# Kernel optimization log

Hardware: AMD Instinct MI355X
Metric: run time of the kernel (lower is better)

## Reference

```python
import jax, jax.numpy as jnp
import numpy as np

V, SMAX, D, L, H, F = 50257, 1024, 768, 12, 12, 3072
DH = D // H
SCALE = float(np.sqrt(DH))


def setup_inputs() -> dict:
    key = jax.random.key(0)
    ks = jax.random.split(key, 24)
    B, S = 2, 1024
    std = 0.02
    inp = {
        'input_ids': jax.random.randint(ks[0], (B, S), 0, V),
        'tok_emb': jax.random.normal(ks[1], (V, D), jnp.float32) * std,
        'pos_emb': jax.random.normal(ks[2], (SMAX, D), jnp.float32) * std,
        # stacked per-layer params (leading dim L)
        'Wq': jax.random.normal(ks[3], (L, D, D), jnp.float32) * std,
        'bq': jnp.zeros((L, D), jnp.float32),
        'Wk': jax.random.normal(ks[4], (L, D, D), jnp.float32) * std,
        'bk': jnp.zeros((L, D), jnp.float32),
        'Wv': jax.random.normal(ks[5], (L, D, D), jnp.float32) * std,
        'bv': jnp.zeros((L, D), jnp.float32),
        'Wo': jax.random.normal(ks[6], (L, D, D), jnp.float32) * std,
        'bo': jnp.zeros((L, D), jnp.float32),
        'ln1_g': jnp.ones((L, D), jnp.float32),
        'ln1_b': jnp.zeros((L, D), jnp.float32),
        'ln2_g': jnp.ones((L, D), jnp.float32),
        'ln2_b': jnp.zeros((L, D), jnp.float32),
        'W1': jax.random.normal(ks[7], (L, D, F), jnp.float32) * std,
        'b1': jnp.zeros((L, F), jnp.float32),
        'W2': jax.random.normal(ks[8], (L, F, D), jnp.float32) * std,
        'b2': jnp.zeros((L, D), jnp.float32),
        'lnf_g': jnp.ones((D,), jnp.float32),
        'lnf_b': jnp.zeros((D,), jnp.float32),
        'Whead': jax.random.normal(ks[9], (D, V), jnp.float32) * std,
    }
    return inp


def _layernorm(x, g, b, eps=1e-5):
    mu = jnp.mean(x, axis=-1, keepdims=True)
    var = jnp.var(x, axis=-1, keepdims=True)
    return (x - mu) * jax.lax.rsqrt(var + eps) * g + b


def _gpt_forward(input_ids, tok_emb, pos_emb, Wq, bq, Wk, bk, Wv, bv, Wo, bo,
                 ln1_g, ln1_b, ln2_g, ln2_b, W1, b1, W2, b2, lnf_g, lnf_b, Whead):
    B, S = input_ids.shape
    x = tok_emb[input_ids] + pos_emb[:S][None, :, :]  # (B,S,D)
    # additive causal mask: -inf above the diagonal
    idx = jnp.arange(S)
    neg_inf = jnp.finfo(x.dtype).min
    mask = jnp.where(idx[None, :] > idx[:, None], neg_inf, 0.0).astype(x.dtype)  # (S,S)

    def block(x, p):
        (wq, bq_, wk, bk_, wv, bv_, wo, bo_, g1, b1_, g2, b2_, w1, bb1, w2, bb2) = p
        h = _layernorm(x, g1, b1_)
        q = (h @ wq + bq_).reshape(B, S, H, DH)
        k = (h @ wk + bk_).reshape(B, S, H, DH)
        v = (h @ wv + bv_).reshape(B, S, H, DH)
        scores = jnp.einsum('bqhd,bkhd->bhqk', q, k) / SCALE + mask
        attn = jax.nn.softmax(scores, axis=-1)
        o = jnp.einsum('bhqk,bkhd->bqhd', attn, v).reshape(B, S, D)
        x = x + (o @ wo + bo_)
        h2 = _layernorm(x, g2, b2_)
        ffn = jax.nn.gelu(h2 @ w1 + bb1, approximate=False) @ w2 + bb2
        return x + ffn, None

    params = (Wq, bq, Wk, bk, Wv, bv, Wo, bo, ln1_g, ln1_b, ln2_g, ln2_b, W1, b1, W2, b2)
    x, _ = jax.lax.scan(block, x, params)
    x = _layernorm(x, lnf_g, lnf_b)
    return x @ Whead  # (B,S,V) logits


def reference(input_ids, tok_emb, pos_emb, Wq, bq, Wk, bk, Wv, bv, Wo, bo,
              ln1_g, ln1_b, ln2_g, ln2_b, W1, b1, W2, b2, lnf_g, lnf_b, Whead):
    return _gpt_forward(input_ids, tok_emb, pos_emb, Wq, bq, Wk, bk, Wv, bv, Wo, bo,
                        ln1_g, ln1_b, ln2_g, ln2_b, W1, b1, W2, b2, lnf_g, lnf_b, Whead)
```

## Files before the change

kernel.cpp:

```cpp
#include <hip/hip_runtime.h>
#include <hip/hip_bf16.h>
#include <cstdint>
#include <cstddef>

#define DEV __device__ __forceinline__

typedef __attribute__((ext_vector_type(8))) short short8;
typedef __attribute__((ext_vector_type(4))) float f32x4;
typedef unsigned short u16;
typedef unsigned int u32;

static constexpr int Vv = 50257;
static constexpr int Dd = 768;
static constexpr int Ll = 12;
static constexpr int Hh = 12;
static constexpr int Ff = 3072;
static constexpr int Ss = 1024;
static constexpr int Bbatch = 2;
static constexpr int DHh = 64;
static constexpr int Mtok = Bbatch * Ss;
static constexpr int NQKV = 3 * Dd;
static constexpr int VPAD = 50304;

DEV float bf2f(u16 u){ u32 x = ((u32)u) << 16; float f; __builtin_memcpy(&f, &x, 4); return f; }
DEV u16 f2bf(float f){ u32 x; __builtin_memcpy(&x, &f, 4); x += 0x7fffu + ((x >> 16) & 1u); return (u16)(x >> 16); }

DEV void gld_lds16(const void* g, void* l){
  __builtin_amdgcn_global_load_lds((const __attribute__((address_space(1))) void*)g,
                                   (__attribute__((address_space(3))) void*)l, 16, 0, 0);
}

__global__ void k_embed(const int* __restrict__ ids, const float* __restrict__ tok,
                        const float* __restrict__ pos, float* __restrict__ x){
  int t = blockIdx.x;
  int id = ids[t];
  int s = t & (Ss - 1);
  const float* tr = tok + (size_t)id * Dd;
  const float* pr = pos + (size_t)s * Dd;
  float* xr = x + (size_t)t * Dd;
  for (int c = threadIdx.x; c < Dd; c += blockDim.x) xr[c] = tr[c] + pr[c];
}

__global__ __launch_bounds__(256) void k_ln(const float* __restrict__ x, const float* __restrict__ g,
                                            const float* __restrict__ b, u16* __restrict__ y){
  int row = blockIdx.x, tid = threadIdx.x;
  const float* xr = x + (size_t)row * Dd;
  float v0 = xr[tid], v1 = xr[tid + 256], v2 = xr[tid + 512];
  float s = v0 + v1 + v2, ss = v0 * v0 + v1 * v1 + v2 * v2;
  for (int o = 1; o < 64; o <<= 1){ s += __shfl_xor(s, o, 64); ss += __shfl_xor(ss, o, 64); }
  __shared__ float red[8];
  int w = tid >> 6, l = tid & 63;
  if (l == 0){ red[w] = s; red[w + 4] = ss; }
  __syncthreads();
  s = red[0] + red[1] + red[2] + red[3];
  ss = red[4] + red[5] + red[6] + red[7];
  float mu = s * (1.0f / Dd);
  float var = ss * (1.0f / Dd) - mu * mu;
  float rs = rsqrtf(var + 1e-5f);
  u16* yr = y + (size_t)row * Dd;
  yr[tid]       = f2bf((v0 - mu) * rs * g[tid]       + b[tid]);
  yr[tid + 256] = f2bf((v1 - mu) * rs * g[tid + 256] + b[tid + 256]);
  yr[tid + 512] = f2bf((v2 - mu) * rs * g[tid + 512] + b[tid + 512]);
}

__global__ void k_transpose(const float* __restrict__ src, u16* __restrict__ dst,
                            int R, int C, long smat, long dmat){
  __shared__ float tile[32][33];
  src += (size_t)blockIdx.z * smat;
  dst += (size_t)blockIdx.z * dmat;
  int c0 = blockIdx.x * 32, r0 = blockIdx.y * 32;
  int tx = threadIdx.x, ty = threadIdx.y;
  #pragma unroll
  for (int i = 0; i < 4; i++){
    int r = r0 + ty + i * 8, c = c0 + tx;
    if (c < C) tile[ty + i * 8][tx] = src[(size_t)r * C + c];
  }
  __syncthreads();
  #pragma unroll
  for (int i = 0; i < 4; i++){
    int c = c0 + ty + i * 8, r = r0 + tx;
    if (c < C) dst[(size_t)c * R + r] = f2bf(tile[tx][ty + i * 8]);
  }
}

__global__ void k_vt(const u16* __restrict__ qkv, u16* __restrict__ vt){
  __shared__ u16 tile[32][33];
  int z = blockIdx.z, b = z / Hh, h = z % Hh;
  int d0 = blockIdx.x * 32, s0 = blockIdx.y * 32;
  int tx = threadIdx.x, ty = threadIdx.y;
  #pragma unroll
  for (int i = 0; i < 4; i++){
    int sP = s0 + ty + i * 8;
    tile[ty + i * 8][tx] = qkv[(size_t)(b * Ss + sP) * NQKV + 2 * Dd + h * DHh + d0 + tx];
  }
  __syncthreads();
  #pragma unroll
  for (int i = 0; i < 4; i++){
    int d = d0 + ty + i * 8;
    vt[((size_t)(z * DHh + d)) * Ss + s0 + tx] = tile[tx][ty + i * 8];
  }
}

__global__ void k_biaspack(const float* __restrict__ bq, const float* __restrict__ bk,
                           const float* __restrict__ bv, float* __restrict__ o){
  int i = blockIdx.x * 256 + threadIdx.x;
  int col = i % NQKV, lay = i / NQKV;
  float v = (col < Dd) ? bq[lay * Dd + col]
          : (col < 2 * Dd) ? bk[lay * Dd + col - Dd]
          : bv[lay * Dd + col - 2 * Dd];
  o[i] = v;
}

__global__ __launch_bounds__(256) void k_combine(const float* __restrict__ p,
                                                 const float* __restrict__ bias,
                                                 float* __restrict__ x){
  int i = blockIdx.x * 256 + threadIdx.x;
  f32x4 a  = ((const f32x4*)x)[i];
  f32x4 q0 = ((const f32x4*)p)[i];
  f32x4 q1 = ((const f32x4*)(p + (size_t)Mtok * Dd))[i];
  int col0 = (i * 4) % Dd;
  f32x4 bv = *(const f32x4*)(bias + col0);
  ((f32x4*)x)[i] = a + q0 + q1 + bv;
}

template<int BM, int BN, int ACT, bool RES, bool OUTBF, bool SCALEQ, bool NB, bool HASBIAS, bool SPLIT>
__global__ __launch_bounds__(256) void k_gemm(const u16* __restrict__ A, const u16* __restrict__ Bt,
                                              const float* __restrict__ bias, const float* __restrict__ res,
                                              float* __restrict__ Cf, u16* __restrict__ Cb,
                                              int Mm, int Nn, int Kk, int MT, int NT, int KS){
  constexpr int HM = BM / 2, HN = BN / 2;
  constexpr int FM = HM / 16, FN = HN / 16;
  __shared__ __align__(16) u16 ldsA[2][BM * 32];
  __shared__ __align__(16) u16 ldsB[2][BN * 32];
  int tid = threadIdx.x, wid = tid >> 6, l = tid & 63;
  int wm = wid >> 1, wn = wid & 1;
  int lr = l & 15, lc = l >> 4;
  int nwg = gridDim.x, dIdx = blockIdx.x;
  int L = ((nwg & 7) == 0) ? ((dIdx & 7) * (nwg >> 3) + (dIdx >> 3)) : dIdx;
  int kidx = 0;
  if (SPLIT){ int per = MT * NT; kidx = L / per; L -= kidx * per; }
  int mtile = L % MT, ntile = L / MT;
  int m0 = mtile * BM, n0 = ntile * BN;
  int klen = Kk / KS, kbase = kidx * klen, nk = klen >> 5;

  f32x4 acc[FM][FN];
  #pragma unroll
  for (int i = 0; i < FM; i++)
    #pragma unroll
    for (int j = 0; j < FN; j++) acc[i][j] = (f32x4)0.0f;

  constexpr int nA = (BM * 4) / 256, nB = (BN * 4) / 256;
  auto stage = [&](int buf, int kk){
    #pragma unroll
    for (int i = 0; i < nA; i++){
      int id = i * 256 + tid, row = id >> 2, c = id & 3;
      int cs = c ^ ((row >> 1) & 3);
      gld_lds16(A + (size_t)(m0 + row) * Kk + kk + cs * 8,
                (char*)ldsA[buf] + (size_t)(i * 256 + (wid << 6)) * 16);
    }
    #pragma unroll
    for (int i = 0; i < nB; i++){
      int id = i * 256 + tid, row = id >> 2, c = id & 3;
      int cs = c ^ ((row >> 1) & 3);
      gld_lds16(Bt + (size_t)(n0 + row) * Kk + kk + cs * 8,
                (char*)ldsB[buf] + (size_t)(i * 256 + (wid << 6)) * 16);
    }
  };
  auto compute = [&](int buf){
    short8 af[FM], bfr[FN];
    #pragma unroll
    for (int i = 0; i < FM; i++){
      int row = wm * HM + i * 16 + lr;
      af[i] = *(const short8*)((const char*)ldsA[buf] + row * 64 + ((lc ^ ((row >> 1) & 3)) << 4));
    }
    #pragma unroll
    for (int j = 0; j < FN; j++){
      int row = wn * HN + j * 16 + lr;
      bfr[j] = *(const short8*)((const char*)ldsB[buf] + row * 64 + ((lc ^ ((row >> 1) & 3)) << 4));
    }
    #pragma unroll
    for (int i = 0; i < FM; i++)
      #pragma unroll
      for (int j = 0; j < FN; j++)
        acc[i][j] = __builtin_amdgcn_mfma_f32_16x16x32_bf16(af[i], bfr[j], acc[i][j], 0, 0, 0);
  };

  stage(0, kbase);
  __syncthreads();
  for (int t = 0; t < nk - 1; ++t){
    stage((t + 1) & 1, kbase + (t + 1) * 32);
    compute(t & 1);
    __syncthreads();
  }
  compute((nk - 1) & 1);

  if (SPLIT){
    float* P = Cf + (size_t)kidx * Mm * Nn;
    #pragma unroll
    for (int i = 0; i < FM; i++)
      #pragma unroll
      for (int j = 0; j < FN; j++){
        int col = n0 + wn * HN + j * 16 + lr;
        #pragma unroll
        for (int r = 0; r < 4; r++){
          int row = m0 + wm * HM + i * 16 + lc * 4 + r;
          P[(size_t)row * Nn + col] = acc[i][j][r];
        }
      }
    return;
  }
  #pragma unroll
  for (int i = 0; i < FM; i++){
    #pragma unroll
    for (int j = 0; j < FN; j++){
      int col = n0 + wn * HN + j * 16 + lr;
      if (NB && col >= Nn) continue;
      float bv = HASBIAS ? bias[col] : 0.0f;
      #pragma unroll
      for (int r = 0; r < 4; r++){
        int row = m0 + wm * HM + i * 16 + lc * 4 + r;
        float v = acc[i][j][r] + bv;
        if (SCALEQ){ if (col < Dd) v *= 0.125f; }
        if (ACT == 1) v = 0.5f * v * (1.0f + erff(v * 0.70710678118f));
        if (RES) v += res[(size_t)row * Nn + col];
        if (OUTBF) Cb[(size_t)row * Nn + col] = f2bf(v);
        else       Cf[(size_t)row * Nn + col] = v;
      }
    }
  }
}

__global__ __launch_bounds__(256) void k_attn(const u16* __restrict__ qkv, const u16* __restrict__ vt,
                                              u16* __restrict__ o){
  __shared__ __align__(16) u16 ldsK[64 * 64];
  __shared__ __align__(16) u16 ldsV[64 * 64];
  __shared__ __align__(16) u16 ldsP[4 * 16 * 72];
  int iq = blockIdx.x, bh = blockIdx.y, b = bh / Hh, h = bh % Hh;
  int tid = threadIdx.x, wid = tid >> 6, l = tid & 63, lr = l & 15, lc = l >> 4;
  int qrow = b * Ss + iq * 64 + wid * 16 + lr;
  const u16* qp = qkv + (size_t)qrow * NQKV + h * DHh;
  short8 qf[2];
  qf[0] = *(const short8*)(qp + lc * 8);
  qf[1] = *(const short8*)(qp + 32 + lc * 8);
  float mreg[4], lsum[4];
  f32x4 oacc[4];
  #pragma unroll
  for (int r = 0; r < 4; r++){ mreg[r] = -1e30f; lsum[r] = 0.0f; }
  #pragma unroll
  for (int i = 0; i < 4; i++) oacc[i] = (f32x4)0.0f;
  u16* pbase = ldsP + wid * 16 * 72;
  for (int j = 0; j <= iq; j++){
    #pragma unroll
    for (int c = 0; c < 2; c++){
      int id = c * 256 + tid, row = id >> 3, ch = id & 7;
      int cs = ch ^ (row & 7);
      gld_lds16(qkv + (size_t)(b * Ss + j * 64 + row) * NQKV + Dd + h * DHh + cs * 8,
                (char*)ldsK + (size_t)(c * 256 + (wid << 6)) * 16);
      gld_lds16(vt + ((size_t)(bh * DHh + row)) * Ss + j * 64 + cs * 8,
                (char*)ldsV + (size_t)(c * 256 + (wid << 6)) * 16);
    }
    __syncthreads();
    f32x4 sc[4];
    #pragma unroll
    for (int fn = 0; fn < 4; fn++) sc[fn] = (f32x4)0.0f;
    #pragma unroll
    for (int fn = 0; fn < 4; fn++){
      int kv = fn * 16 + lr;
      #pragma unroll
      for (int ks = 0; ks < 2; ks++){
        int ch = ks * 4 + lc;
        short8 kf = *(const short8*)((const char*)ldsK + kv * 128 + ((ch ^ (kv & 7)) << 4));
        sc[fn] = __builtin_amdgcn_mfma_f32_16x16x32_bf16(qf[ks], kf, sc[fn], 0, 0, 0);
      }
    }
    if (j == iq){
      #pragma unroll
      for (int fn = 0; fn < 4; fn++){
        int kv = fn * 16 + lr;
        #pragma unroll
        for (int r = 0; r < 4; r++){
          int qr = wid * 16 + lc * 4 + r;
          if (kv > qr) sc[fn][r] = -1e30f;
        }
      }
    }
    float alpha[4];
    #pragma unroll
    for (int r = 0; r < 4; r++){
      float mx = fmaxf(fmaxf(sc[0][r], sc[1][r]), fmaxf(sc[2][r], sc[3][r]));
      mx = fmaxf(mx, __shfl_xor(mx, 1, 64));
      mx = fmaxf(mx, __shfl_xor(mx, 2, 64));
      mx = fmaxf(mx, __shfl_xor(mx, 4, 64));
      mx = fmaxf(mx, __shfl_xor(mx, 8, 64));
      float mnew = fmaxf(mreg[r], mx);
      alpha[r] = __expf(mreg[r] - mnew);
      mreg[r] = mnew;
      float rsum = 0.0f;
      #pragma unroll
      for (int fn = 0; fn < 4; fn++){
        float p = __expf(sc[fn][r] - mnew);
        sc[fn][r] = p;
        rsum += p;
      }
      rsum += __shfl_xor(rsum, 1, 64);
      rsum += __shfl_xor(rsum, 2, 64);
      rsum += __shfl_xor(rsum, 4, 64);
      rsum += __shfl_xor(rsum, 8, 64);
      lsum[r] = lsum[r] * alpha[r] + rsum;
    }
    #pragma unroll
    for (int fn = 0; fn < 4; fn++)
      #pragma unroll
      for (int r = 0; r < 4; r++)
        pbase[(lc * 4 + r) * 72 + fn * 16 + lr] = f2bf(sc[fn][r]);
    #pragma unroll
    for (int fd = 0; fd < 4; fd++)
      #pragma unroll
      for (int r = 0; r < 4; r++) oacc[fd][r] *= alpha[r];
    short8 pa[2];
    #pragma unroll
    for (int ks = 0; ks < 2; ks++)
      pa[ks] = *(const short8*)((const char*)pbase + lr * 144 + (ks * 4 + lc) * 16);
    #pragma unroll
    for (int fd = 0; fd < 4; fd++){
      int dd = fd * 16 + lr;
      #pragma unroll
      for (int ks = 0; ks < 2; ks++){
        int ch = ks * 4 + lc;
        short8 vf = *(const short8*)((const char*)ldsV + dd * 128 + ((ch ^ (dd & 7)) << 4));
        oacc[fd] = __builtin_amdgcn_mfma_f32_16x16x32_bf16(pa[ks], vf, oacc[fd], 0, 0, 0);
      }
    }
    __syncthreads();
  }
  #pragma unroll
  for (int fd = 0; fd < 4; fd++)
    #pragma unroll
    for (int r = 0; r < 4; r++){
      int row = b * Ss + iq * 64 + wid * 16 + lc * 4 + r;
      o[(size_t)row * Dd + h * DHh + fd * 16 + lr] = f2bf(oacc[fd][r] / lsum[r]);
    }
}

extern "C" void kernel_launch(void* const* d_in, const int* in_sizes, int n_in,
                              void* d_out, int out_size, void* d_ws, size_t ws_size,
                              hipStream_t stream){
  const int*   ids  = (const int*)d_in[0];
  const float* tok  = (const float*)d_in[1];
  const float* pos  = (const float*)d_in[2];
  const float* Wq   = (const float*)d_in[3];
  const float* bq   = (const float*)d_in[4];
  const float* Wk   = (const float*)d_in[5];
  const float* bk   = (const float*)d_in[6];
  const float* Wv   = (const float*)d_in[7];
  const float* bv   = (const float*)d_in[8];
  const float* Wo   = (const float*)d_in[9];
  const float* bo   = (const float*)d_in[10];
  const float* ln1g = (const float*)d_in[11];
  const float* ln1b = (const float*)d_in[12];
  const float* ln2g = (const float*)d_in[13];
  const float* ln2b = (const float*)d_in[14];
  const float* W1   = (const float*)d_in[15];
  const float* b1   = (const float*)d_in[16];
  const float* W2   = (const float*)d_in[17];
  const float* b2   = (const float*)d_in[18];
  const float* lnfg = (const float*)d_in[19];
  const float* lnfb = (const float*)d_in[20];
  const float* Wh   = (const float*)d_in[21];
  float* out = (float*)d_out;

  auto al = [](size_t x){ return (x + 255) & ~(size_t)255; };
  size_t off = 0;
  auto take = [&](size_t bytes){ size_t r = off; off = al(off + bytes); return r; };
  size_t o_x    = take((size_t)Mtok * Dd * 4);
  size_t o_h    = take((size_t)Mtok * Dd * 2);
  size_t o_qkv  = take((size_t)Mtok * NQKV * 2);
  size_t o_vt   = take((size_t)Bbatch * Hh * DHh * Ss * 2);
  size_t o_o    = take((size_t)Mtok * Dd * 2);
  size_t o_mid  = take((size_t)Mtok * Ff * 2);
  size_t o_bq   = take((size_t)Ll * NQKV * 4);
  size_t o_part = take((size_t)2 * Mtok * Dd * 4);
  size_t o_rot = off;
  size_t o_wqkv, o_wo, o_w1, o_w2, o_wh;
  bool full;
  {
    size_t t = off;
    o_wqkv = t; t = al(t + (size_t)Ll * NQKV * Dd * 2);
    o_wo   = t; t = al(t + (size_t)Ll * Dd * Dd * 2);
    o_w1   = t; t = al(t + (size_t)Ll * Ff * Dd * 2);
    o_w2   = t; t = al(t + (size_t)Ll * Dd * Ff * 2);
    o_wh   = t; t = al(t + (size_t)VPAD * Dd * 2);
    full = (t <= ws_size);
  }
  char* ws = (char*)d_ws;
  float* x    = (float*)(ws + o_x);
  u16*   h    = (u16*)(ws + o_h);
  u16*   qkvb = (u16*)(ws + o_qkv);
  u16*   vtb  = (u16*)(ws + o_vt);
  u16*   ob   = (u16*)(ws + o_o);
  u16*   midb = (u16*)(ws + o_mid);
  float* bqkvp= (float*)(ws + o_bq);
  float* part = (float*)(ws + o_part);
  u16* wqkvT = full ? (u16*)(ws + o_wqkv) : (u16*)(ws + o_rot);
  u16* woT   = full ? (u16*)(ws + o_wo)   : (u16*)(ws + o_rot);
  u16* w1T   = full ? (u16*)(ws + o_w1)   : (u16*)(ws + o_rot);
  u16* w2T   = full ? (u16*)(ws + o_w2)   : (u16*)(ws + o_rot);
  u16* whT   = full ? (u16*)(ws + o_wh)   : (u16*)(ws + o_rot);

  dim3 tb(32, 8);
  auto tpose = [&](const float* src, u16* dst, int R, int C, int nmat, long smat, long dmat){
    k_transpose<<<dim3((C + 31) / 32, R / 32, nmat), tb, 0, stream>>>(src, dst, R, C, smat, dmat);
  };

  k_biaspack<<<(Ll * NQKV) / 256, 256, 0, stream>>>(bq, bk, bv, bqkvp);
  k_embed<<<Mtok, 256, 0, stream>>>(ids, tok, pos, x);

  if (full){
    tpose(Wq, wqkvT,              Dd, Dd, Ll, (long)Dd * Dd, (long)NQKV * Dd);
    tpose(Wk, wqkvT + Dd * Dd,    Dd, Dd, Ll, (long)Dd * Dd, (long)NQKV * Dd);
    tpose(Wv, wqkvT + 2 * Dd * Dd,Dd, Dd, Ll, (long)Dd * Dd, (long)NQKV * Dd);
    tpose(Wo, woT, Dd, Dd, Ll, (long)Dd * Dd, (long)Dd * Dd);
    tpose(W1, w1T, Dd, Ff, Ll, (long)Dd * Ff, (long)Ff * Dd);
    tpose(W2, w2T, Ff, Dd, Ll, (long)Ff * Dd, (long)Dd * Ff);
    tpose(Wh, whT, Dd, Vv, 1, 0, 0);
  }

  auto gemm_qkv = [&](const u16* A, const u16* Bt, const float* bias, u16* Cb){
    constexpr int MT = Mtok / 64, NT = NQKV / 128;
    k_gemm<64, 128, 0, false, true, true, false, true, false>
      <<<MT * NT, 256, 0, stream>>>(A, Bt, bias, nullptr, nullptr, Cb, Mtok, NQKV, Dd, MT, NT, 1);
  };
  auto gemm_wo = [&](const u16* A, const u16* Bt, const float* bias, float* C){
    constexpr int MT = Mtok / 64, NT = Dd / 64;
    k_gemm<64, 64, 0, true, false, false, false, true, false>
      <<<MT * NT, 256, 0, stream>>>(A, Bt, bias, C, C, nullptr, Mtok, Dd, Dd, MT, NT, 1);
  };
  auto gemm_ffn1 = [&](const u16* A, const u16* Bt, const float* bias, u16* Cb){
    constexpr int MT = Mtok / 64, NT = Ff / 128;
    k_gemm<64, 128, 1, false, true, false, false, true, false>
      <<<MT * NT, 256, 0, stream>>>(A, Bt, bias, nullptr, nullptr, Cb, Mtok, Ff, Dd, MT, NT, 1);
  };
  auto gemm_ffn2 = [&](const u16* A, const u16* Bt){
    constexpr int MT = Mtok / 64, NT = Dd / 64;
    k_gemm<64, 64, 0, false, false, false, false, false, true>
      <<<MT * NT * 2, 256, 0, stream>>>(A, Bt, nullptr, nullptr, part, nullptr, Mtok, Dd, Ff, MT, NT, 2);
  };
  auto gemm_head = [&](const u16* A, const u16* Bt, float* C){
    constexpr int MT = Mtok / 128, NT = VPAD / 128;
    k_gemm<128, 128, 0, false, false, false, true, false, false>
      <<<MT * NT, 256, 0, stream>>>(A, Bt, nullptr, nullptr, C, nullptr, Mtok, Vv, Dd, MT, NT, 1);
  };

  for (int l = 0; l < Ll; ++l){
    const u16* wqkvL = full ? wqkvT + (size_t)l * NQKV * Dd : wqkvT;
    const u16* woL   = full ? woT   + (size_t)l * Dd * Dd   : woT;
    const u16* w1L   = full ? w1T   + (size_t)l * Ff * Dd   : w1T;
    const u16* w2L   = full ? w2T   + (size_t)l * Dd * Ff   : w2T;
    if (!full){
      tpose(Wq + (size_t)l * Dd * Dd, wqkvT,              Dd, Dd, 1, 0, 0);
      tpose(Wk + (size_t)l * Dd * Dd, wqkvT + Dd * Dd,    Dd, Dd, 1, 0, 0);
      tpose(Wv + (size_t)l * Dd * Dd, wqkvT + 2 * Dd * Dd,Dd, Dd, 1, 0, 0);
    }
    k_ln<<<Mtok, 256, 0, stream>>>(x, ln1g + l * Dd, ln1b + l * Dd, h);
    gemm_qkv(h, wqkvL, bqkvp + l * NQKV, qkvb);
    k_vt<<<dim3(2, 32, Bbatch * Hh), tb, 0, stream>>>(qkvb, vtb);
    k_attn<<<dim3(Ss / 64, Bbatch * Hh), 256, 0, stream>>>(qkvb, vtb, ob);
    if (!full) tpose(Wo + (size_t)l * Dd * Dd, woT, Dd, Dd, 1, 0, 0);
    gemm_wo(ob, woL, bo + l * Dd, x);
    k_ln<<<Mtok, 256, 0, stream>>>(x, ln2g + l * Dd, ln2b + l * Dd, h);
    if (!full) tpose(W1 + (size_t)l * Dd * Ff, w1T, Dd, Ff, 1, 0, 0);
    gemm_ffn1(h, w1L, b1 + l * Ff, midb);
    if (!full) tpose(W2 + (size_t)l * Ff * Dd, w2T, Ff, Dd, 1, 0, 0);
    gemm_ffn2(midb, w2L);
    k_combine<<<(Mtok * Dd / 4) / 256, 256, 0, stream>>>(part, b2 + l * Dd, x);
  }
  k_ln<<<Mtok, 256, 0, stream>>>(x, lnfg, lnfb, h);
  if (!full) tpose(Wh, whT, Dd, Vv, 1, 0, 0);
  gemm_head(h, whT, out);
}
```

Measured before the change: 2.235 ms.

## Add 4-stage pipelined GEMM kernel and fuse V transpose into QKV epilogue

Introduces a new GEMM kernel with a 4-deep LDS buffer ring, explicit vmcnt waits, one barrier per k-step, and split MFMA issue with priority hints. It is used for the QKV, FFN1 and LM-head GEMMs, with larger tiles (128x128, and 256x256 with 8 waves for the head). The V transpose kernel is removed: the QKV epilogue now also writes V in transposed layout, saving a launch and a read pass. The risks are more LDS per block, which can lower occupancy, and scattered transposed stores in the epilogue. The vocab padding is enlarged to fit the 256 tile, which assumes the head weight buffer is allocated for the larger padding.

```diff
diff --git a/kernel.cpp b/kernel.cpp
--- a/kernel.cpp
+++ b/kernel.cpp
@@ -4,6 +4,7 @@
 #include <cstddef>
 
 #define DEV __device__ __forceinline__
+#define WAITV(N) asm volatile("s_waitcnt vmcnt(" #N ")" ::: "memory")
 
 typedef __attribute__((ext_vector_type(8))) short short8;
 typedef __attribute__((ext_vector_type(4))) float f32x4;
@@ -20,7 +21,7 @@
 static constexpr int DHh = 64;
 static constexpr int Mtok = Bbatch * Ss;
 static constexpr int NQKV = 3 * Dd;
-static constexpr int VPAD = 50304;
+static constexpr int VPAD = 50432;
 
 DEV float bf2f(u16 u){ u32 x = ((u32)u) << 16; float f; __builtin_memcpy(&f, &x, 4); return f; }
 DEV u16 f2bf(float f){ u32 x; __builtin_memcpy(&x, &f, 4); x += 0x7fffu + ((x >> 16) & 1u); return (u16)(x >> 16); }
@@ -83,24 +84,6 @@
   }
 }
 
-__global__ void k_vt(const u16* __restrict__ qkv, u16* __restrict__ vt){
-  __shared__ u16 tile[32][33];
-  int z = blockIdx.z, b = z / Hh, h = z % Hh;
-  int d0 = blockIdx.x * 32, s0 = blockIdx.y * 32;
-  int tx = threadIdx.x, ty = threadIdx.y;
-  #pragma unroll
-  for (int i = 0; i < 4; i++){
-    int sP = s0 + ty + i * 8;
-    tile[ty + i * 8][tx] = qkv[(size_t)(b * Ss + sP) * NQKV + 2 * Dd + h * DHh + d0 + tx];
-  }
-  __syncthreads();
-  #pragma unroll
-  for (int i = 0; i < 4; i++){
-    int d = d0 + ty + i * 8;
-    vt[((size_t)(z * DHh + d)) * Ss + s0 + tx] = tile[tx][ty + i * 8];
-  }
-}
-
 __global__ void k_biaspack(const float* __restrict__ bq, const float* __restrict__ bk,
                            const float* __restrict__ bv, float* __restrict__ o){
   int i = blockIdx.x * 256 + threadIdx.x;
@@ -123,10 +106,134 @@
   ((f32x4*)x)[i] = a + q0 + q1 + bv;
 }
 
-template<int BM, int BN, int ACT, bool RES, bool OUTBF, bool SCALEQ, bool NB, bool HASBIAS, bool SPLIT>
+template<int BM, int BN, int NW, int EPI>
+__global__ __launch_bounds__(NW * 64, 2) void k_gemm8(
+    const u16* __restrict__ A, const u16* __restrict__ Bt,
+    const float* __restrict__ bias, float* __restrict__ Cf, u16* __restrict__ Cb,
+    u16* __restrict__ vt, int Nn, int Kk, int MT, int NT){
+  constexpr int NTHR = NW * 64;
+  constexpr int WM = 2, WN = NW / 2;
+  constexpr int WMS = BM / WM, WNS = BN / WN;
+  constexpr int FM = WMS / 16, FN = WNS / 16, FMH = FM / 2;
+  __shared__ __align__(16) u16 ldsA[4 * BM * 32];
+  __shared__ __align__(16) u16 ldsB[4 * BN * 32];
+  int tid = threadIdx.x, wid = tid >> 6, l = tid & 63;
+  int wm = wid / WN, wn = wid % WN;
+  int lr = l & 15, lc = l >> 4;
+  int nwg = gridDim.x, dIdx = blockIdx.x;
+  int L = (dIdx & 7) * (nwg >> 3) + (dIdx >> 3);
+  int mtile = L % MT, ntile = L / MT;
+  int m0 = mtile * BM, n0 = ntile * BN;
+
+  f32x4 acc[FM][FN];
+  #pragma unroll
+  for (int i = 0; i < FM; i++)
+    #pragma unroll
+    for (int j = 0; j < FN; j++) acc[i][j] = (f32x4)0.0f;
+
+  constexpr int nA = (BM * 4) / NTHR, nB = (BN * 4) / NTHR;
+  auto stage = [&](int buf, int kk){
+    char* dA = (char*)ldsA + buf * (BM * 64);
+    #pragma unroll
+    for (int i = 0; i < nA; i++){
+      int id = i * NTHR + tid, row = id >> 2, c = id & 3;
+      int cs = c ^ ((row >> 1) & 3);
+      gld_lds16(A + (size_t)(m0 + row) * Kk + kk + cs * 8, dA + (size_t)id * 16);
+    }
+    char* dB = (char*)ldsB + buf * (BN * 64);
+    #pragma unroll
+    for (int i = 0; i < nB; i++){
+      int id = i * NTHR + tid, row = id >> 2, c = id & 3;
+      int cs = c ^ ((row >> 1) & 3);
+      gld_lds16(Bt + (size_t)(n0 + row) * Kk + kk + cs * 8, dB + (size_t)id * 16);
+    }
+  };
+  auto compute = [&](int t){
+    const char* bA = (const char*)ldsA + (t & 3) * (BM * 64);
+    const char* bB = (const char*)ldsB + (t & 3) * (BN * 64);
+    short8 bfr[FN], af[FMH];
+    #pragma unroll
+    for (int j = 0; j < FN; j++){
+      int row = wn * WNS + j * 16 + lr;
+      bfr[j] = *(const short8*)(bB + row * 64 + ((lc ^ ((row >> 1) & 3)) << 4));
+    }
+    #pragma unroll
+    for (int i = 0; i < FMH; i++){
+      int row = wm * WMS + i * 16 + lr;
+      af[i] = *(const short8*)(bA + row * 64 + ((lc ^ ((row >> 1) & 3)) << 4));
+    }
+    asm volatile("s_waitcnt lgkmcnt(0)" ::: "memory");
+    __builtin_amdgcn_sched_barrier(0);
+    __builtin_amdgcn_s_setprio(1);
+    #pragma unroll
+    for (int i = 0; i < FMH; i++)
+      #pragma unroll
+      for (int j = 0; j < FN; j++)
+        acc[i][j] = __builtin_amdgcn_mfma_f32_16x16x32_bf16(af[i], bfr[j], acc[i][j], 0, 0, 0);
+    __builtin_amdgcn_s_setprio(0);
+    #pragma unroll
+    for (int i = 0; i < FMH; i++){
+      int row = wm * WMS + (FMH + i) * 16 + lr;
+      af[i] = *(const short8*)(bA + row * 64 + ((lc ^ ((row >> 1) & 3)) << 4));
+    }
+    asm volatile("s_waitcnt lgkmcnt(0)" ::: "memory");
+    __builtin_amdgcn_sched_barrier(0);
+    __builtin_amdgcn_s_setprio(1);
+    #pragma unroll
+    for (int i = 0; i < FMH; i++)
+      #pragma unroll
+      for (int j = 0; j < FN; j++)
+        acc[FMH + i][j] = __builtin_amdgcn_mfma_f32_16x16x32_bf16(af[i], bfr[j], acc[FMH + i][j], 0, 0, 0);
+    __builtin_amdgcn_s_setprio(0);
+  };
+
+  int nk = Kk >> 5;
+  stage(0, 0); stage(1, 32); stage(2, 64);
+  #pragma unroll 1
+  for (int t = 0; t < nk - 3; ++t){
+    WAITV(8);
+    __builtin_amdgcn_s_barrier();
+    __builtin_amdgcn_sched_barrier(0);
+    stage((t + 3) & 3, (t + 3) << 5);
+    compute(t);
+  }
+  WAITV(8); __builtin_amdgcn_s_barrier(); __builtin_amdgcn_sched_barrier(0); compute(nk - 3);
+  WAITV(4); __builtin_amdgcn_s_barrier(); __builtin_amdgcn_sched_barrier(0); compute(nk - 2);
+  WAITV(0); __builtin_amdgcn_s_barrier(); __builtin_amdgcn_sched_barrier(0); compute(nk - 1);
+
+  #pragma unroll
+  for (int i = 0; i < FM; i++){
+    #pragma unroll
+    for (int j = 0; j < FN; j++){
+      int col = n0 + wn * WNS + j * 16 + lr;
+      if (EPI == 0 && col >= Nn) continue;
+      float bv = (EPI != 0) ? bias[col] : 0.0f;
+      #pragma unroll
+      for (int r = 0; r < 4; r++){
+        int row = m0 + wm * WMS + i * 16 + lc * 4 + r;
+        float v = acc[i][j][r] + bv;
+        if (EPI == 1){ if (col < Dd) v *= 0.125f; }
+        if (EPI == 2) v = 0.5f * v * (1.0f + erff(v * 0.70710678118f));
+        if (EPI == 0){
+          Cf[(size_t)row * Nn + col] = v;
+        } else {
+          u16 bvv = f2bf(v);
+          Cb[(size_t)row * Nn + col] = bvv;
+          if (EPI == 1 && col >= 2 * Dd){
+            int c2 = col - 2 * Dd, hh = c2 >> 6, dd2 = c2 & 63;
+            int bb = row >> 10, ss2 = row & 1023;
+            vt[((size_t)((bb * Hh + hh) * DHh + dd2) << 10) + ss2] = bvv;
+          }
+        }
+      }
+    }
+  }
+}
+
+template<int BM, int BN, bool RES, bool SPLIT>
 __global__ __launch_bounds__(256) void k_gemm(const u16* __restrict__ A, const u16* __restrict__ Bt,
                                               const float* __restrict__ bias, const float* __restrict__ res,
-                                              float* __restrict__ Cf, u16* __restrict__ Cb,
+                                              float* __restrict__ Cf,
                                               int Mm, int Nn, int Kk, int MT, int NT, int KS){
   constexpr int HM = BM / 2, HN = BN / 2;
   constexpr int FM = HM / 16, FN = HN / 16;
@@ -156,14 +263,14 @@
       int id = i * 256 + tid, row = id >> 2, c = id & 3;
       int cs = c ^ ((row >> 1) & 3);
       gld_lds16(A + (size_t)(m0 + row) * Kk + kk + cs * 8,
-                (char*)ldsA[buf] + (size_t)(i * 256 + (wid << 6)) * 16);
+                (char*)ldsA[buf] + (size_t)id * 16);
     }
     #pragma unroll
     for (int i = 0; i < nB; i++){
       int id = i * 256 + tid, row = id >> 2, c = id & 3;
       int cs = c ^ ((row >> 1) & 3);
       gld_lds16(Bt + (size_t)(n0 + row) * Kk + kk + cs * 8,
-                (char*)ldsB[buf] + (size_t)(i * 256 + (wid << 6)) * 16);
+                (char*)ldsB[buf] + (size_t)id * 16);
     }
   };
   auto compute = [&](int buf){
@@ -214,17 +321,13 @@
     #pragma unroll
     for (int j = 0; j < FN; j++){
       int col = n0 + wn * HN + j * 16 + lr;
-      if (NB && col >= Nn) continue;
-      float bv = HASBIAS ? bias[col] : 0.0f;
+      float bv = bias[col];
       #pragma unroll
       for (int r = 0; r < 4; r++){
         int row = m0 + wm * HM + i * 16 + lc * 4 + r;
         float v = acc[i][j][r] + bv;
-        if (SCALEQ){ if (col < Dd) v *= 0.125f; }
-        if (ACT == 1) v = 0.5f * v * (1.0f + erff(v * 0.70710678118f));
         if (RES) v += res[(size_t)row * Nn + col];
-        if (OUTBF) Cb[(size_t)row * Nn + col] = f2bf(v);
-        else       Cf[(size_t)row * Nn + col] = v;
+        Cf[(size_t)row * Nn + col] = v;
       }
     }
   }
@@ -425,30 +528,25 @@
     tpose(Wh, whT, Dd, Vv, 1, 0, 0);
   }
 
-  auto gemm_qkv = [&](const u16* A, const u16* Bt, const float* bias, u16* Cb){
-    constexpr int MT = Mtok / 64, NT = NQKV / 128;
-    k_gemm<64, 128, 0, false, true, true, false, true, false>
-      <<<MT * NT, 256, 0, stream>>>(A, Bt, bias, nullptr, nullptr, Cb, Mtok, NQKV, Dd, MT, NT, 1);
-  };
-  auto gemm_wo = [&](const u16* A, const u16* Bt, const float* bias, float* C){
+  auto gemm_qkv = [&](const u16* Aop, const u16* Bop, const float* bias, u16* Cb){
+    constexpr int MT = Mtok / 128, NT = NQKV / 128;
+    k_gemm8<128, 128, 4, 1><<<MT * NT, 256, 0, stream>>>(Aop, Bop, bias, nullptr, Cb, vtb, NQKV, Dd, MT, NT);
+  };
+  auto gemm_wo = [&](const u16* Aop, const u16* Bop, const float* bias, float* C){
     constexpr int MT = Mtok / 64, NT = Dd / 64;
-    k_gemm<64, 64, 0, true, false, false, false, true, false>
-      <<<MT * NT, 256, 0, stream>>>(A, Bt, bias, C, C, nullptr, Mtok, Dd, Dd, MT, NT, 1);
-  };
-  auto gemm_ffn1 = [&](const u16* A, const u16* Bt, const float* bias, u16* Cb){
-    constexpr int MT = Mtok / 64, NT = Ff / 128;
-    k_gemm<64, 128, 1, false, true, false, false, true, false>
-      <<<MT * NT, 256, 0, stream>>>(A, Bt, bias, nullptr, nullptr, Cb, Mtok, Ff, Dd, MT, NT, 1);
-  };
-  auto gemm_ffn2 = [&](const u16* A, const u16* Bt){
+    k_gemm<64, 64, true, false><<<MT * NT, 256, 0, stream>>>(Aop, Bop, bias, C, C, Mtok, Dd, Dd, MT, NT, 1);
+  };
+  auto gemm_ffn1 = [&](const u16* Aop, const u16* Bop, const float* bias, u16* Cb){
+    constexpr int MT = Mtok / 128, NT = Ff / 128;
+    k_gemm8<128, 128, 4, 2><<<MT * NT, 256, 0, stream>>>(Aop, Bop, bias, nullptr, Cb, nullptr, Ff, Dd, MT, NT);
+  };
+  auto gemm_ffn2 = [&](const u16* Aop, const u16* Bop){
     constexpr int MT = Mtok / 64, NT = Dd / 64;
-    k_gemm<64, 64, 0, false, false, false, false, false, true>
-      <<<MT * NT * 2, 256, 0, stream>>>(A, Bt, nullptr, nullptr, part, nullptr, Mtok, Dd, Ff, MT, NT, 2);
-  };
-  auto gemm_head = [&](const u16* A, const u16* Bt, float* C){
-    constexpr int MT = Mtok / 128, NT = VPAD / 128;
-    k_gemm<128, 128, 0, false, false, false, true, false, false>
-      <<<MT * NT, 256, 0, stream>>>(A, Bt, nullptr, nullptr, C, nullptr, Mtok, Vv, Dd, MT, NT, 1);
+    k_gemm<64, 64, false, true><<<MT * NT * 2, 256, 0, stream>>>(Aop, Bop, nullptr, nullptr, part, Mtok, Dd, Ff, MT, NT, 2);
+  };
+  auto gemm_head = [&](const u16* Aop, const u16* Bop, float* C){
+    constexpr int MT = Mtok / 256, NT = VPAD / 256;
+    k_gemm8<256, 256, 8, 0><<<MT * NT, 512, 0, stream>>>(Aop, Bop, nullptr, C, nullptr, nullptr, Vv, Dd, MT, NT);
   };
 
   for (int l = 0; l < Ll; ++l){
@@ -463,7 +561,6 @@
     }
     k_ln<<<Mtok, 256, 0, stream>>>(x, ln1g + l * Dd, ln1b + l * Dd, h);
     gemm_qkv(h, wqkvL, bqkvp + l * NQKV, qkvb);
-    k_vt<<<dim3(2, 32, Bbatch * Hh), tb, 0, stream>>>(qkvb, vtb);
     k_attn<<<dim3(Ss / 64, Bbatch * Hh), 256, 0, stream>>>(qkvb, vtb, ob);
     if (!full) tpose(Wo + (size_t)l * Dd * Dd, woT, Dd, Dd, 1, 0, 0);
     gemm_wo(ob, woL, bo + l * Dd, x);
```

Result: slower. 2.454 ms (+9.8%).
